# Kernel tuning notes

Measured on AMD Instinct MI355X. Metric: run time of the kernel, lower is better.

## Reference

```python
import jax, jax.numpy as jnp
import numpy as np

B, T, D, H, DFF = 64, 100, 1024, 16, 4096
HD = D // H
EPS = 1e-5


def _rope_tables(t_len, hd, dtype):
    # matches RotaryEmbedding: inv_freq over even dims, emb = cat([freqs, freqs])
    inv_freq = 1.0 / (10000.0 ** (jnp.arange(0, hd, 2, dtype=jnp.float32) / hd))
    t = jnp.arange(t_len, dtype=jnp.float32)
    freqs = jnp.einsum('i,j->ij', t, inv_freq)          # (T, hd/2)
    emb = jnp.concatenate([freqs, freqs], axis=-1)      # (T, hd)
    # apply_rope uses cos[..., ::2] / sin[..., ::2]
    cos = jnp.cos(emb)[:, ::2].astype(dtype)            # (T, hd/2)
    sin = jnp.sin(emb)[:, ::2].astype(dtype)
    return cos, sin


def _apply_rope(x, cos, sin):
    # x: (B, H, T, hd); cos/sin: (T, hd/2) broadcast over B,H
    x1 = x[..., ::2]
    x2 = x[..., 1::2]
    return jnp.concatenate([x1 * cos - x2 * sin, x1 * sin + x2 * cos], axis=-1)


def _layernorm(x, g, b):
    mu = jnp.mean(x, axis=-1, keepdims=True)
    var = jnp.mean(jnp.square(x - mu), axis=-1, keepdims=True)
    return (x - mu) * jax.lax.rsqrt(var + EPS) * g + b


def setup_inputs() -> dict:
    key = jax.random.key(0)
    ks = jax.random.split(key, 8)
    s = 0.02
    return {
        'tgt': jax.random.normal(ks[0], (B, T, D), dtype=jnp.float32),
        'Wqkv': jax.random.normal(ks[1], (3 * D, D), dtype=jnp.float32) * s,
        'bqkv': jnp.zeros((3 * D,), jnp.float32),
        'Wo': jax.random.normal(ks[2], (D, D), dtype=jnp.float32) * s,
        'bo': jnp.zeros((D,), jnp.float32),
        'W1': jax.random.normal(ks[3], (DFF, D), dtype=jnp.float32) * s,
        'b1': jnp.zeros((DFF,), jnp.float32),
        'W2': jax.random.normal(ks[4], (D, DFF), dtype=jnp.float32) * s,
        'b2': jnp.zeros((D,), jnp.float32),
        'g1': jnp.ones((D,), jnp.float32),
        'be1': jnp.zeros((D,), jnp.float32),
        'g2': jnp.ones((D,), jnp.float32),
        'be2': jnp.zeros((D,), jnp.float32),
        'tgt_mask': jnp.tril(jnp.ones((T, T), jnp.int32)),
    }


def reference(tgt, Wqkv, bqkv, Wo, bo, W1, b1, W2, b2, g1, be1, g2, be2, tgt_mask):
    dtype = tgt.dtype
    # QKV projection (torch Linear: x @ W.T + b)
    qkv = jnp.einsum('btd,ed->bte', tgt, Wqkv) + bqkv          # (B,T,3D)
    qkv = qkv.reshape(B, T, 3, H, HD).transpose(2, 0, 3, 1, 4)  # (3,B,H,T,hd)
    q, k, v = qkv[0], qkv[1], qkv[2]

    cos, sin = _rope_tables(T, HD, dtype)
    q = _apply_rope(q, cos, sin)
    k = _apply_rope(k, cos, sin)

    scale = 1.0 / np.sqrt(HD)
    scores = jnp.einsum('bhqd,bhkd->bhqk', q, k) * scale        # (B,H,T,T)
    scores = jnp.where(tgt_mask == 0, -jnp.inf, scores)
    attn = jax.nn.softmax(scores, axis=-1)
    ctx = jnp.einsum('bhqk,bhkd->bhqd', attn, v)                # (B,H,T,hd)
    ctx = ctx.transpose(0, 2, 1, 3).reshape(B, T, D)

    tgt2 = jnp.einsum('btd,ed->bte', ctx, Wo) + bo
    x = _layernorm(tgt + tgt2, g1, be1)

    h = jax.nn.relu(jnp.einsum('btd,fd->btf', x, W1) + b1)
    ff = jnp.einsum('btf,df->btd', h, W2) + b2
    out = _layernorm(x + ff, g2, be2)
    return out
```

## Files before the change

kernel.cpp:

```cpp
#include <hip/hip_runtime.h>
#include <math.h>

#define Bn   64
#define Tn   100
#define Tp   128
#define Dn   1024
#define Hn   16
#define HDn  64
#define DFFn 4096
#define EPSf 1e-5f

typedef unsigned short ushort_t;
typedef __attribute__((ext_vector_type(8))) __bf16 bf16x8;
typedef __attribute__((ext_vector_type(4))) float f32x4;

__device__ __forceinline__ float u2f(ushort_t u) {
    union { unsigned int i; float f; } v; v.i = ((unsigned int)u) << 16; return v.f;
}
__device__ __forceinline__ ushort_t f2bf(float f) {
    union { float f; unsigned int u; } v; v.f = f;
    unsigned int r = v.u + 0x7FFFu + ((v.u >> 16) & 1u);
    return (ushort_t)(r >> 16);
}

__device__ __forceinline__ void gload_lds16(const void* g, void* l) {
    __builtin_amdgcn_global_load_lds(
        (const __attribute__((address_space(1))) unsigned int*)g,
        (__attribute__((address_space(3))) unsigned int*)l,
        16, 0, 0);
}

struct ConvSeg { const float* src; ushort_t* dst; int n4; };
struct Conv5   { ConvSeg seg[5]; };

__global__ __launch_bounds__(256) void conv_bf16_multi(Conv5 cfg)
{
    int i = blockIdx.x * 256 + threadIdx.x;
    #pragma unroll
    for (int s = 0; s < 5; ++s) {
        const int n = cfg.seg[s].n4;
        if (i < n) {
            float4 v = ((const float4*)cfg.seg[s].src)[i];
            ushort4 o;
            o.x = f2bf(v.x); o.y = f2bf(v.y); o.z = f2bf(v.z); o.w = f2bf(v.w);
            ((ushort4*)cfg.seg[s].dst)[i] = o;
            return;
        }
        i -= n;
    }
}

#define GEMM_TILE_MAP(gx_, gy_, swz_)                                        \
    const int L  = blockIdx.x;                                               \
    int rowt, colt;                                                          \
    if (swz_) {                                                              \
        const int group = L / (8 * (gx_));                                   \
        int l = L - group * 8 * (gx_);                                       \
        const int rem = (gy_) - group * 8;                                   \
        if (rem >= 8) { rowt = group * 8 + (l & 7); colt = l >> 3; }         \
        else          { rowt = group * 8 + l % rem; colt = l / rem; }        \
    } else { rowt = L / (gx_); colt = L - rowt * (gx_); }

#define GEMM_KLOOP(A_, B_, K_)                                               \
    for (int k0 = 0; k0 < (K_); k0 += 64) {                                  \
        __syncthreads();                                                     \
        _Pragma("unroll")                                                    \
        for (int t = 0; t < 4; ++t) {                                        \
            const int idx = (wave * 4 + t) * 64 + lane;                      \
            const int row = idx >> 3;                                        \
            const int gc  = (idx & 7) ^ (row & 7);                           \
            gload_lds16((A_) + (size_t)(row0 + row) * (K_) + k0 + gc * 8,    \
                        &As[idx * 8]);                                       \
            gload_lds16((B_) + (size_t)(col0 + row) * (K_) + k0 + gc * 8,    \
                        &Bs[idx * 8]);                                       \
        }                                                                    \
        __syncthreads();                                                     \
        _Pragma("unroll")                                                    \
        for (int kh = 0; kh < 2; ++kh) {                                     \
            const int chunk = kh * 4 + g;                                    \
            bf16x8 af[4], bfr[4];                                            \
            _Pragma("unroll")                                                \
            for (int i = 0; i < 4; ++i) {                                    \
                const int ra = wrow + i * 16 + frow;                         \
                af[i]  = *(const bf16x8*)&As[ra * 64 + (chunk ^ (ra & 7)) * 8]; \
                const int rb = wcol + i * 16 + frow;                         \
                bfr[i] = *(const bf16x8*)&Bs[rb * 64 + (chunk ^ (rb & 7)) * 8]; \
            }                                                                \
            _Pragma("unroll")                                                \
            for (int i = 0; i < 4; ++i)                                      \
                _Pragma("unroll")                                            \
                for (int j = 0; j < 4; ++j)                                  \
                    acc[i][j] = __builtin_amdgcn_mfma_f32_16x16x32_bf16(     \
                        af[i], bfr[j], acc[i][j], 0, 0, 0);                  \
        }                                                                    \
    }

template<bool RELU, bool ADDRES, typename OutT>
__global__ __launch_bounds__(256) void gemm_bt_mfma(const ushort_t* __restrict__ A,
                                                    const ushort_t* __restrict__ Bm,
                                                    const float* __restrict__ bias,
                                                    const ushort_t* __restrict__ res,
                                                    OutT* __restrict__ C,
                                                    int M, int N, int K,
                                                    int gx, int swz)
{
    __shared__ __align__(16) ushort_t As[128 * 64];
    __shared__ __align__(16) ushort_t Bs[128 * 64];

    const int gy = M >> 7;
    GEMM_TILE_MAP(gx, gy, swz)

    const int tid  = threadIdx.x;
    const int wave = tid >> 6;
    const int lane = tid & 63;
    const int row0 = rowt * 128;
    const int col0 = colt * 128;
    const int wrow = (wave >> 1) * 64;
    const int wcol = (wave & 1) * 64;
    const int frow = lane & 15;
    const int g    = lane >> 4;

    f32x4 acc[4][4] = {};
    GEMM_KLOOP(A, Bm, K)

    const int crow = (lane >> 4) * 4;
    const int ccol = lane & 15;
    #pragma unroll
    for (int i = 0; i < 4; ++i) {
        #pragma unroll
        for (int r = 0; r < 4; ++r) {
            const int row = row0 + wrow + i * 16 + crow + r;
            #pragma unroll
            for (int j = 0; j < 4; ++j) {
                const int col = col0 + wcol + j * 16 + ccol;
                float v = acc[i][j][r] + bias[col];
                if (ADDRES) v += u2f(res[(size_t)row * N + col]);
                if (RELU) v = fmaxf(v, 0.f);
                if constexpr (sizeof(OutT) == 2)
                    C[(size_t)row * N + col] = (OutT)f2bf(v);
                else
                    C[(size_t)row * N + col] = (OutT)v;
            }
        }
    }
}

__global__ __launch_bounds__(256) void gemm_qkv_rope(const ushort_t* __restrict__ A,
                                                     const ushort_t* __restrict__ Bm,
                                                     const float* __restrict__ bias,
                                                     ushort_t* __restrict__ q,
                                                     ushort_t* __restrict__ k,
                                                     ushort_t* __restrict__ vt)
{
    __shared__ __align__(16) ushort_t As[128 * 64];
    __shared__ __align__(16) ushort_t Bs[128 * 64];

    const int gy = 50, gx = 24;
    GEMM_TILE_MAP(gx, gy, 1)

    const int tid  = threadIdx.x;
    const int wave = tid >> 6;
    const int lane = tid & 63;
    const int row0 = rowt * 128;
    const int col0 = colt * 128;
    const int wrow = (wave >> 1) * 64;
    const int wcol = (wave & 1) * 64;
    const int frow = lane & 15;
    const int g    = lane >> 4;

    f32x4 acc[4][4] = {};
    GEMM_KLOOP(A, Bm, Dn)

    const int sec = col0 >> 10;

    __syncthreads();
    float2* tab = (float2*)As;
    if (sec != 2) {
        for (int e = tid; e < 2048; e += 256) {
            const int lr = e >> 4, f = e & 15;
            const int row = row0 + lr;
            const int b = row / Tn;
            const int t = row - b * Tn;
            float s, c;
            sincosf((float)t * exp2f(-0.83048202f * (float)f), &s, &c);
            tab[lr * 16 + f] = make_float2(c, s);
        }
    }
    __syncthreads();

    const int crow = (lane >> 4) * 4;
    const int ccol = lane & 15;

    if (sec == 2) {
        #pragma unroll
        for (int i = 0; i < 4; ++i) {
            #pragma unroll
            for (int r = 0; r < 4; ++r) {
                const int row = row0 + wrow + i * 16 + crow + r;
                const int b = row / Tn, t = row - b * Tn;
                #pragma unroll
                for (int j = 0; j < 4; ++j) {
                    const int colg = col0 + wcol + j * 16 + ccol;
                    const int hcol = colg & 1023;
                    const int h = hcol >> 6, d = hcol & 63;
                    const float v = acc[i][j][r] + bias[colg];
                    vt[((size_t)(b * Hn + h) * HDn + d) * Tp + t] = f2bf(v);
                }
            }
        }
    } else {
        ushort_t* dst = sec ? k : q;
        const int odd = ccol & 1;
        const int f0  = ccol >> 1;
        #pragma unroll
        for (int i = 0; i < 4; ++i) {
            #pragma unroll
            for (int r = 0; r < 4; ++r) {
                const int lr  = wrow + i * 16 + crow + r;
                const int row = row0 + lr;
                const int b = row / Tn, t = row - b * Tn;
                const float2 cs0 = tab[lr * 16 + f0];
                const float2 cs1 = tab[lr * 16 + 8 + f0];
                (void)t;
                #pragma unroll
                for (int j = 0; j < 4; ++j) {
                    const int colg = col0 + wcol + j * 16 + ccol;
                    const int hcol = colg & 1023;
                    const int h  = hcol >> 6;
                    const int dh = hcol & 63;
                    const int m  = dh >> 1;
                    const float val   = acc[i][j][r] + bias[colg];
                    const float other = __shfl_xor(val, 1);
                    const float sn = (j & 1) ? cs1.y : cs0.y;
                    const float cs = (j & 1) ? cs1.x : cs0.x;
                    const float x1 = odd ? other : val;
                    const float x2 = odd ? val : other;
                    const float o  = odd ? (x1 * sn + x2 * cs)
                                         : (x1 * cs - x2 * sn);
                    const int outcol = odd ? (m + 32) : m;
                    dst[((size_t)(b * Hn + h) * Tp + t) * HDn + outcol] = f2bf(o);
                }
            }
        }
    }
}

__global__ __launch_bounds__(256) void attn_mfma(const ushort_t* __restrict__ q,
                                                 const ushort_t* __restrict__ k,
                                                 const ushort_t* __restrict__ vt,
                                                 ushort_t* __restrict__ ctx)
{
    __shared__ __align__(16) ushort_t sm[24576];

    const int bh   = blockIdx.x;
    const int b    = bh >> 4, h = bh & 15;
    const int tid  = threadIdx.x;
    const int wave = tid >> 6;
    const int lane = tid & 63;
    const int c    = lane & 15;
    const int g    = lane >> 4;
    const int R0   = wave * 32;

    const ushort_t* qg = q  + (size_t)bh * Tp * HDn;
    const ushort_t* kg = k  + (size_t)bh * Tp * HDn;
    const ushort_t* vg = vt + (size_t)bh * HDn * Tp;
    for (int s = wave; s < 16; s += 4) {
        const int idx = s * 64 + lane;
        { const int row = idx >> 3, pc = idx & 7, gc = pc ^ (row & 7);
          gload_lds16(qg + row * 64 + gc * 8, &sm[idx * 8]);
          gload_lds16(kg + row * 64 + gc * 8, &sm[8192 + idx * 8]); }
        { const int row = idx >> 4, pc = idx & 15, gc = pc ^ (row & 15);
          gload_lds16(vg + row * 128 + gc * 8, &sm[16384 + idx * 8]); }
    }
    __syncthreads();

    f32x4 acc[2][8] = {};
    #pragma unroll
    for (int ks = 0; ks < 2; ++ks) {
        const int cb = ks * 4;
        bf16x8 aq[2];
        #pragma unroll
        for (int i = 0; i < 2; ++i) {
            const int row = R0 + i * 16 + c;
            const int ph  = (cb + g) ^ (row & 7);
            aq[i] = *(const bf16x8*)&sm[row * 64 + ph * 8];
        }
        #pragma unroll
        for (int j = 0; j < 8; ++j) {
            const int row = j * 16 + c;
            const int ph  = (cb + g) ^ (row & 7);
            const bf16x8 bk = *(const bf16x8*)&sm[8192 + row * 64 + ph * 8];
            acc[0][j] = __builtin_amdgcn_mfma_f32_16x16x32_bf16(aq[0], bk, acc[0][j], 0, 0, 0);
            acc[1][j] = __builtin_amdgcn_mfma_f32_16x16x32_bf16(aq[1], bk, acc[1][j], 0, 0, 0);
        }
    }
    __syncthreads();

    float linv[2][4];
    #pragma unroll
    for (int i = 0; i < 2; ++i) {
        #pragma unroll
        for (int r = 0; r < 4; ++r) {
            const int row = R0 + i * 16 + g * 4 + r;
            float sv[8], m = -1e30f;
            #pragma unroll
            for (int j = 0; j < 8; ++j) {
                const int col = j * 16 + c;
                const float s = acc[i][j][r] * 0.125f;
                sv[j] = (col <= row) ? s : -1e30f;
                m = fmaxf(m, sv[j]);
            }
            #pragma unroll
            for (int msk = 1; msk < 16; msk <<= 1) m = fmaxf(m, __shfl_xor(m, msk));
            float l = 0.f;
            #pragma unroll
            for (int j = 0; j < 8; ++j) {
                const int col = j * 16 + c;
                const float p = (col <= row) ? __expf(sv[j] - m) : 0.f;
                sv[j] = p; l += p;
            }
            #pragma unroll
            for (int msk = 1; msk < 16; msk <<= 1) l += __shfl_xor(l, msk);
            linv[i][r] = 1.f / l;
            #pragma unroll
            for (int j = 0; j < 8; ++j) {
                const int chunk = j * 2 + (c >> 3);
                const int ph    = chunk ^ (row & 15);
                sm[row * 128 + ph * 8 + (c & 7)] = f2bf(sv[j]);
            }
        }
    }
    __syncthreads();

    f32x4 acc2[2][4] = {};
    #pragma unroll
    for (int ks = 0; ks < 4; ++ks) {
        const int cb = ks * 4;
        bf16x8 ap[2];
        #pragma unroll
        for (int i = 0; i < 2; ++i) {
            const int row = R0 + i * 16 + c;
            const int ph  = (cb + g) ^ (row & 15);
            ap[i] = *(const bf16x8*)&sm[row * 128 + ph * 8];
        }
        #pragma unroll
        for (int n = 0; n < 4; ++n) {
            const int row = n * 16 + c;
            const int ph  = (cb + g) ^ (row & 15);
            const bf16x8 bv = *(const bf16x8*)&sm[16384 + row * 128 + ph * 8];
            acc2[0][n] = __builtin_amdgcn_mfma_f32_16x16x32_bf16(ap[0], bv, acc2[0][n], 0, 0, 0);
            acc2[1][n] = __builtin_amdgcn_mfma_f32_16x16x32_bf16(ap[1], bv, acc2[1][n], 0, 0, 0);
        }
    }

    #pragma unroll
    for (int i = 0; i < 2; ++i) {
        #pragma unroll
        for (int r = 0; r < 4; ++r) {
            const int row = R0 + i * 16 + g * 4 + r;
            if (row < Tn) {
                const float s = linv[i][r];
                #pragma unroll
                for (int n = 0; n < 4; ++n) {
                    const int col = n * 16 + c;
                    ctx[(size_t)(b * Tn + row) * Dn + h * HDn + col] =
                        f2bf(acc2[i][n][r] * s);
                }
            }
        }
    }
}

__global__ __launch_bounds__(256) void ln_single(const ushort_t* __restrict__ a,
                                                 const float* __restrict__ g,
                                                 const float* __restrict__ be,
                                                 ushort_t* __restrict__ out_bf)
{
    const int row = blockIdx.x;
    const int tid = threadIdx.x;
    __shared__ float red[256];
    const size_t base = (size_t)row * Dn;

    float vals[4];
    float s = 0.f;
    #pragma unroll
    for (int i = 0; i < 4; ++i) {
        const int c = tid + i * 256;
        vals[i] = u2f(a[base + c]);
        s += vals[i];
    }
    red[tid] = s;
    __syncthreads();
    for (int o = 128; o > 0; o >>= 1) {
        if (tid < o) red[tid] += red[tid + o];
        __syncthreads();
    }
    const float mu = red[0] * (1.f / Dn);
    __syncthreads();

    float vs = 0.f;
    #pragma unroll
    for (int i = 0; i < 4; ++i) { const float d = vals[i] - mu; vs += d * d; }
    red[tid] = vs;
    __syncthreads();
    for (int o = 128; o > 0; o >>= 1) {
        if (tid < o) red[tid] += red[tid + o];
        __syncthreads();
    }
    const float rstd = rsqrtf(red[0] * (1.f / Dn) + EPSf);

    #pragma unroll
    for (int i = 0; i < 4; ++i) {
        const int c = tid + i * 256;
        out_bf[base + c] = f2bf((vals[i] - mu) * rstd * g[c] + be[c]);
    }
}

__global__ __launch_bounds__(256) void add_ln2(const ushort_t* __restrict__ a,
                                               const ushort_t* __restrict__ r,
                                               const float* __restrict__ g,
                                               const float* __restrict__ be,
                                               float* __restrict__ out)
{
    const int row = blockIdx.x;
    const int tid = threadIdx.x;
    __shared__ float red[256];
    const size_t base = (size_t)row * Dn;

    float vals[4];
    float s = 0.f;
    #pragma unroll
    for (int i = 0; i < 4; ++i) {
        const int c = tid + i * 256;
        vals[i] = u2f(a[base + c]) + u2f(r[base + c]);
        s += vals[i];
    }
    red[tid] = s;
    __syncthreads();
    for (int o = 128; o > 0; o >>= 1) {
        if (tid < o) red[tid] += red[tid + o];
        __syncthreads();
    }
    const float mu = red[0] * (1.f / Dn);
    __syncthreads();

    float vs = 0.f;
    #pragma unroll
    for (int i = 0; i < 4; ++i) { const float d = vals[i] - mu; vs += d * d; }
    red[tid] = vs;
    __syncthreads();
    for (int o = 128; o > 0; o >>= 1) {
        if (tid < o) red[tid] += red[tid + o];
        __syncthreads();
    }
    const float rstd = rsqrtf(red[0] * (1.f / Dn) + EPSf);

    #pragma unroll
    for (int i = 0; i < 4; ++i) {
        const int c = tid + i * 256;
        out[base + c] = (vals[i] - mu) * rstd * g[c] + be[c];
    }
}

extern "C" void kernel_launch(void* const* d_in, const int* in_sizes, int n_in,
                              void* d_out, int out_size, void* d_ws, size_t ws_size,
                              hipStream_t stream)
{
    const float* tgt  = (const float*)d_in[0];
    const float* Wqkv = (const float*)d_in[1];
    const float* bqkv = (const float*)d_in[2];
    const float* Wo   = (const float*)d_in[3];
    const float* bo   = (const float*)d_in[4];
    const float* W1   = (const float*)d_in[5];
    const float* b1   = (const float*)d_in[6];
    const float* W2   = (const float*)d_in[7];
    const float* b2   = (const float*)d_in[8];
    const float* g1   = (const float*)d_in[9];
    const float* be1  = (const float*)d_in[10];
    const float* g2   = (const float*)d_in[11];
    const float* be2  = (const float*)d_in[12];
    float* out = (float*)d_out;
    (void)in_sizes; (void)n_in; (void)out_size; (void)ws_size;

    const int M = Bn * Tn;

    char* w = (char*)d_ws;
    ushort_t* tgt_bf  = (ushort_t*)(w);
    ushort_t* Wqkv_bf = (ushort_t*)(w + 13107200);
    ushort_t* Wo_bf   = (ushort_t*)(w + 19398656);
    ushort_t* W1_bf   = (ushort_t*)(w + 21495808);
    ushort_t* W2_bf   = (ushort_t*)(w + 29884416);

    ushort_t* qb    = (ushort_t*)(w + 38273024);
    ushort_t* kb    = (ushort_t*)(w + 55050240);
    ushort_t* vtb   = (ushort_t*)(w + 71827456);
    ushort_t* hbuf  = (ushort_t*)(w + 38273024);
    ushort_t* ctxb  = (ushort_t*)(w + 88604672);
    ushort_t* tgt2b = (ushort_t*)(w + 101711872);
    ushort_t* ffb   = (ushort_t*)(w + 101711872);
    ushort_t* x_bf  = (ushort_t*)(w + 114819072);

    Conv5 cfg;
    cfg.seg[0] = { tgt,  tgt_bf,  M * Dn / 4 };
    cfg.seg[1] = { Wqkv, Wqkv_bf, 3 * Dn * Dn / 4 };
    cfg.seg[2] = { Wo,   Wo_bf,   Dn * Dn / 4 };
    cfg.seg[3] = { W1,   W1_bf,   DFFn * Dn / 4 };
    cfg.seg[4] = { W2,   W2_bf,   Dn * DFFn / 4 };
    const int total4 = (M * Dn + 3 * Dn * Dn + Dn * Dn + 2 * DFFn * Dn) / 4;
    conv_bf16_multi<<<(total4 + 255) / 256, 256, 0, stream>>>(cfg);

    gemm_qkv_rope<<<1200, 256, 0, stream>>>(tgt_bf, Wqkv_bf, bqkv, qb, kb, vtb);
    attn_mfma<<<Bn * Hn, 256, 0, stream>>>(qb, kb, vtb, ctxb);
    gemm_bt_mfma<false, true, ushort_t><<<(Dn / 128) * (M / 128), 256, 0, stream>>>(
        ctxb, Wo_bf, bo, tgt_bf, tgt2b, M, Dn, Dn, Dn / 128, 1);
    ln_single<<<M, 256, 0, stream>>>(tgt2b, g1, be1, x_bf);
    gemm_bt_mfma<true, false, ushort_t><<<(DFFn / 128) * (M / 128), 256, 0, stream>>>(
        x_bf, W1_bf, b1, nullptr, hbuf, M, DFFn, Dn, DFFn / 128, 0);
    gemm_bt_mfma<false, false, ushort_t><<<(Dn / 128) * (M / 128), 256, 0, stream>>>(
        hbuf, W2_bf, b2, nullptr, ffb, M, Dn, DFFn, Dn / 128, 1);
    add_ln2<<<M, 256, 0, stream>>>(x_bf, ffb, g2, be2, out);
}
```

Measured before the change: 440.8 us.

## Add 256x256-tile double-buffered MFMA GEMM for QKV+RoPE and FFN1

Introduces a 512-thread GEMM with a 256x256 output tile. It uses double-buffered LDS with XOR-swizzled layout and direct global-to-LDS loads. The next K-slices are staged between MFMA quarter-steps, with explicit waitcnt, barriers and raised wave priority during the MFMA bursts. The QKV+RoPE GEMM and the W1 (ReLU) GEMM switch to this kernel to raise data reuse per tile and overlap loads with compute. In exchange, there are far fewer blocks (300 and 400), which risks tail-wave imbalance on the CUs, and each block needs 128KB of LDS, which limits occupancy.

```diff
diff --git a/kernel.cpp b/kernel.cpp
--- a/kernel.cpp
+++ b/kernel.cpp
@@ -145,38 +145,165 @@
     }
 }
 
-__global__ __launch_bounds__(256) void gemm_qkv_rope(const ushort_t* __restrict__ A,
+#define STAGE_HALF(SRC, ROWBASE, LD, LDSBASE)                                \
+    { _Pragma("unroll")                                                      \
+      for (int i_ = 0; i_ < 2; ++i_) {                                       \
+          const int idx_ = i_ * 512 + tid;                                   \
+          const int row_ = idx_ >> 3;                                        \
+          const int gc_  = (idx_ & 7) ^ (row_ & 7);                          \
+          gload_lds16((SRC) + (size_t)((ROWBASE) + row_) * (LD) + gc_ * 8,   \
+                      (LDSBASE) + idx_ * 8);                                 \
+      } }
+
+#define GEMM256_KLOOP(A_, B_, K_)                                            \
+    const int NT_ = (K_) >> 6;                                               \
+    STAGE_HALF((B_),      col0,       (K_), &Bs[0][0])                       \
+    STAGE_HALF((B_),      col0 + 128, (K_), &Bs[0][128 * 64])                \
+    STAGE_HALF((A_),      row0,       (K_), &As[0][0])                       \
+    STAGE_HALF((A_),      row0 + 128, (K_), &As[0][128 * 64])                \
+    STAGE_HALF((B_) + 64, col0,       (K_), &Bs[1][0])                       \
+    STAGE_HALF((B_) + 64, col0 + 128, (K_), &Bs[1][128 * 64])                \
+    asm volatile("s_waitcnt vmcnt(4)" ::: "memory");                         \
+    __builtin_amdgcn_s_barrier();                                            \
+    for (int t_ = 0; t_ < NT_; ++t_) {                                       \
+        const int  buf_ = t_ & 1;                                            \
+        const bool stA_ = (t_ + 1 < NT_);                                    \
+        const bool stB_ = (t_ + 2 < NT_);                                    \
+        bf16x8 bfr_[4][2];                                                   \
+        _Pragma("unroll")                                                    \
+        for (int q_ = 0; q_ < 4; ++q_) {                                     \
+            bf16x8 af_[2][2];                                                \
+            _Pragma("unroll")                                                \
+            for (int ii_ = 0; ii_ < 2; ++ii_)                                \
+                _Pragma("unroll")                                            \
+                for (int kk_ = 0; kk_ < 2; ++kk_) {                          \
+                    const int ra_ = wm * 128 + (2 * q_ + ii_) * 16 + frow;   \
+                    const int ch_ = kk_ * 4 + g;                             \
+                    af_[ii_][kk_] = *(const bf16x8*)                         \
+                        &As[buf_][ra_ * 64 + ((ch_ ^ (ra_ & 7))) * 8];       \
+                }                                                            \
+            if (q_ == 0) {                                                   \
+                _Pragma("unroll")                                            \
+                for (int j_ = 0; j_ < 4; ++j_)                               \
+                    _Pragma("unroll")                                        \
+                    for (int kk_ = 0; kk_ < 2; ++kk_) {                      \
+                        const int rb_ = wn * 64 + j_ * 16 + frow;            \
+                        const int ch_ = kk_ * 4 + g;                         \
+                        bfr_[j_][kk_] = *(const bf16x8*)                     \
+                            &Bs[buf_][rb_ * 64 + ((ch_ ^ (rb_ & 7))) * 8];   \
+                    }                                                        \
+            }                                                                \
+            if (q_ == 0 && stA_)                                             \
+                STAGE_HALF((A_) + (t_ + 1) * 64, row0,       (K_), &As[buf_ ^ 1][0]) \
+            if (q_ == 1 && stA_)                                             \
+                STAGE_HALF((A_) + (t_ + 1) * 64, row0 + 128, (K_), &As[buf_ ^ 1][128 * 64]) \
+            if (q_ == 2 && stB_)                                             \
+                STAGE_HALF((B_) + (t_ + 2) * 64, col0,       (K_), &Bs[buf_][0]) \
+            if (q_ == 3 && stB_)                                             \
+                STAGE_HALF((B_) + (t_ + 2) * 64, col0 + 128, (K_), &Bs[buf_][128 * 64]) \
+            __builtin_amdgcn_s_barrier();                                    \
+            asm volatile("s_waitcnt lgkmcnt(0)" ::: "memory");               \
+            __builtin_amdgcn_sched_barrier(0);                               \
+            __builtin_amdgcn_s_setprio(1);                                   \
+            _Pragma("unroll")                                                \
+            for (int ii_ = 0; ii_ < 2; ++ii_)                                \
+                _Pragma("unroll")                                            \
+                for (int j_ = 0; j_ < 4; ++j_)                               \
+                    _Pragma("unroll")                                        \
+                    for (int kk_ = 0; kk_ < 2; ++kk_)                        \
+                        acc[2 * q_ + ii_][j_] =                              \
+                            __builtin_amdgcn_mfma_f32_16x16x32_bf16(         \
+                                af_[ii_][kk_], bfr_[j_][kk_],                \
+                                acc[2 * q_ + ii_][j_], 0, 0, 0);             \
+            __builtin_amdgcn_s_setprio(0);                                   \
+            __builtin_amdgcn_sched_barrier(0);                               \
+            if (q_ == 3) {                                                   \
+                if (stB_)      asm volatile("s_waitcnt vmcnt(4)" ::: "memory"); \
+                else if (stA_) asm volatile("s_waitcnt vmcnt(0)" ::: "memory"); \
+            }                                                                \
+            __builtin_amdgcn_s_barrier();                                    \
+        }                                                                    \
+    }
+
+template<bool RELU, typename OutT>
+__global__ __launch_bounds__(512, 2) void gemm256_bt(const ushort_t* __restrict__ A,
                                                      const ushort_t* __restrict__ Bm,
                                                      const float* __restrict__ bias,
-                                                     ushort_t* __restrict__ q,
-                                                     ushort_t* __restrict__ k,
-                                                     ushort_t* __restrict__ vt)
-{
-    __shared__ __align__(16) ushort_t As[128 * 64];
-    __shared__ __align__(16) ushort_t Bs[128 * 64];
-
-    const int gy = 50, gx = 24;
-    GEMM_TILE_MAP(gx, gy, 1)
+                                                     OutT* __restrict__ C,
+                                                     int M, int N, int K,
+                                                     int gx, int swz)
+{
+    __shared__ __align__(16) ushort_t As[2][256 * 64];
+    __shared__ __align__(16) ushort_t Bs[2][256 * 64];
+
+    const int gy = M >> 8;
+    GEMM_TILE_MAP(gx, gy, swz)
 
     const int tid  = threadIdx.x;
+    const int lane = tid & 63;
     const int wave = tid >> 6;
-    const int lane = tid & 63;
-    const int row0 = rowt * 128;
-    const int col0 = colt * 128;
-    const int wrow = (wave >> 1) * 64;
-    const int wcol = (wave & 1) * 64;
+    const int wm   = wave >> 2;
+    const int wn   = wave & 3;
+    const int row0 = rowt * 256;
+    const int col0 = colt * 256;
     const int frow = lane & 15;
     const int g    = lane >> 4;
 
-    f32x4 acc[4][4] = {};
-    GEMM_KLOOP(A, Bm, Dn)
+    f32x4 acc[8][4] = {};
+    GEMM256_KLOOP(A, Bm, K)
+
+    const int crow = (lane >> 4) * 4;
+    const int ccol = lane & 15;
+    #pragma unroll
+    for (int i = 0; i < 8; ++i) {
+        #pragma unroll
+        for (int r = 0; r < 4; ++r) {
+            const int row = row0 + wm * 128 + i * 16 + crow + r;
+            #pragma unroll
+            for (int j = 0; j < 4; ++j) {
+                const int col = col0 + wn * 64 + j * 16 + ccol;
+                float v = acc[i][j][r] + bias[col];
+                if (RELU) v = fmaxf(v, 0.f);
+                if constexpr (sizeof(OutT) == 2)
+                    C[(size_t)row * N + col] = (OutT)f2bf(v);
+                else
+                    C[(size_t)row * N + col] = (OutT)v;
+            }
+        }
+    }
+}
+
+__global__ __launch_bounds__(512, 2) void gemm256_qkv_rope(const ushort_t* __restrict__ A,
+                                                           const ushort_t* __restrict__ Bm,
+                                                           const float* __restrict__ bias,
+                                                           ushort_t* __restrict__ q,
+                                                           ushort_t* __restrict__ k,
+                                                           ushort_t* __restrict__ vt)
+{
+    __shared__ __align__(16) ushort_t As[2][256 * 64];
+    __shared__ __align__(16) ushort_t Bs[2][256 * 64];
+
+    const int gy = 25, gx = 12;
+    GEMM_TILE_MAP(gx, gy, 1)
+
+    const int tid  = threadIdx.x;
+    const int lane = tid & 63;
+    const int wave = tid >> 6;
+    const int wm   = wave >> 2;
+    const int wn   = wave & 3;
+    const int row0 = rowt * 256;
+    const int col0 = colt * 256;
+    const int frow = lane & 15;
+    const int g    = lane >> 4;
+
+    f32x4 acc[8][4] = {};
+    GEMM256_KLOOP(A, Bm, Dn)
 
     const int sec = col0 >> 10;
 
-    __syncthreads();
-    float2* tab = (float2*)As;
+    float2* tab = (float2*)&As[0][0];
     if (sec != 2) {
-        for (int e = tid; e < 2048; e += 256) {
+        for (int e = tid; e < 4096; e += 512) {
             const int lr = e >> 4, f = e & 15;
             const int row = row0 + lr;
             const int b = row / Tn;
@@ -193,14 +320,14 @@
 
     if (sec == 2) {
         #pragma unroll
-        for (int i = 0; i < 4; ++i) {
+        for (int i = 0; i < 8; ++i) {
             #pragma unroll
             for (int r = 0; r < 4; ++r) {
-                const int row = row0 + wrow + i * 16 + crow + r;
+                const int row = row0 + wm * 128 + i * 16 + crow + r;
                 const int b = row / Tn, t = row - b * Tn;
                 #pragma unroll
                 for (int j = 0; j < 4; ++j) {
-                    const int colg = col0 + wcol + j * 16 + ccol;
+                    const int colg = col0 + wn * 64 + j * 16 + ccol;
                     const int hcol = colg & 1023;
                     const int h = hcol >> 6, d = hcol & 63;
                     const float v = acc[i][j][r] + bias[colg];
@@ -213,18 +340,17 @@
         const int odd = ccol & 1;
         const int f0  = ccol >> 1;
         #pragma unroll
-        for (int i = 0; i < 4; ++i) {
+        for (int i = 0; i < 8; ++i) {
             #pragma unroll
             for (int r = 0; r < 4; ++r) {
-                const int lr  = wrow + i * 16 + crow + r;
+                const int lr  = wm * 128 + i * 16 + crow + r;
                 const int row = row0 + lr;
                 const int b = row / Tn, t = row - b * Tn;
                 const float2 cs0 = tab[lr * 16 + f0];
                 const float2 cs1 = tab[lr * 16 + 8 + f0];
-                (void)t;
                 #pragma unroll
                 for (int j = 0; j < 4; ++j) {
-                    const int colg = col0 + wcol + j * 16 + ccol;
+                    const int colg = col0 + wn * 64 + j * 16 + ccol;
                     const int hcol = colg & 1023;
                     const int h  = hcol >> 6;
                     const int dh = hcol & 63;
@@ -509,13 +635,13 @@
     const int total4 = (M * Dn + 3 * Dn * Dn + Dn * Dn + 2 * DFFn * Dn) / 4;
     conv_bf16_multi<<<(total4 + 255) / 256, 256, 0, stream>>>(cfg);
 
-    gemm_qkv_rope<<<1200, 256, 0, stream>>>(tgt_bf, Wqkv_bf, bqkv, qb, kb, vtb);
+    gemm256_qkv_rope<<<25 * 12, 512, 0, stream>>>(tgt_bf, Wqkv_bf, bqkv, qb, kb, vtb);
     attn_mfma<<<Bn * Hn, 256, 0, stream>>>(qb, kb, vtb, ctxb);
     gemm_bt_mfma<false, true, ushort_t><<<(Dn / 128) * (M / 128), 256, 0, stream>>>(
         ctxb, Wo_bf, bo, tgt_bf, tgt2b, M, Dn, Dn, Dn / 128, 1);
     ln_single<<<M, 256, 0, stream>>>(tgt2b, g1, be1, x_bf);
-    gemm_bt_mfma<true, false, ushort_t><<<(DFFn / 128) * (M / 128), 256, 0, stream>>>(
-        x_bf, W1_bf, b1, nullptr, hbuf, M, DFFn, Dn, DFFn / 128, 0);
+    gemm256_bt<true, ushort_t><<<(M / 256) * (DFFn / 256), 512, 0, stream>>>(
+        x_bf, W1_bf, b1, hbuf, M, DFFn, Dn, DFFn / 256, 0);
     gemm_bt_mfma<false, false, ushort_t><<<(Dn / 128) * (M / 128), 256, 0, stream>>>(
         hbuf, W2_bf, b2, nullptr, ffb, M, Dn, DFFn, Dn / 128, 1);
     add_ln2<<<M, 256, 0, stream>>>(x_bf, ffb, g2, be2, out);
```

Result: slower. 482.2 us (+9.4%).

## Replace 128x128 GEMMs with 256-row double-buffered 512-thread MFMA kernel

Applied to the files above, without the earlier changes.

Replaces the generic 128x128-tile GEMM used for the output projection and both FFN matmuls with a 512-thread kernel that computes 256xBN tiles (BN=128 or 256). It double-buffers LDS, issuing global-to-LDS loads for the next K slices in stages interleaved with MFMA work, and uses manual vmcnt waits, barriers and setprio. Larger tiles raise arithmetic intensity and cut redundant global loads, and the prefetch schedule is meant to hide memory latency. In exchange it uses more LDS and registers per block and launches fewer blocks, so occupancy and load balance may suffer on small grids such as the 1024-wide GEMMs. The hand-tuned wait counts must also match the number of loads in flight.

```diff
diff --git a/kernel.cpp b/kernel.cpp
--- a/kernel.cpp
+++ b/kernel.cpp
@@ -29,6 +29,9 @@
         (__attribute__((address_space(3))) unsigned int*)l,
         16, 0, 0);
 }
+
+#define VMWAIT_(n) asm volatile("s_waitcnt vmcnt(" #n ")" ::: "memory")
+#define VMWAIT(n)  VMWAIT_(n)
 
 struct ConvSeg { const float* src; ushort_t* dst; int n4; };
 struct Conv5   { ConvSeg seg[5]; };
@@ -95,47 +98,129 @@
         }                                                                    \
     }
 
-template<bool RELU, bool ADDRES, typename OutT>
-__global__ __launch_bounds__(256) void gemm_bt_mfma(const ushort_t* __restrict__ A,
-                                                    const ushort_t* __restrict__ Bm,
-                                                    const float* __restrict__ bias,
-                                                    const ushort_t* __restrict__ res,
-                                                    OutT* __restrict__ C,
-                                                    int M, int N, int K,
-                                                    int gx, int swz)
+template<int BN, bool RELU, bool ADDRES, typename OutT>
+__global__ __launch_bounds__(512, 2) void gemm256_bt(const ushort_t* __restrict__ A,
+                                                     const ushort_t* __restrict__ Bm,
+                                                     const float* __restrict__ bias,
+                                                     const ushort_t* __restrict__ res,
+                                                     OutT* __restrict__ C,
+                                                     int M, int N, int K,
+                                                     int gx, int swz)
 {
-    __shared__ __align__(16) ushort_t As[128 * 64];
-    __shared__ __align__(16) ushort_t Bs[128 * 64];
-
-    const int gy = M >> 7;
+    constexpr int JN = BN / 64;
+    constexpr int NB = BN / 128;
+    __shared__ __align__(16) ushort_t As[2][256 * 64];
+    __shared__ __align__(16) ushort_t Bs[2][BN * 64];
+
+    const int gy = M >> 8;
     GEMM_TILE_MAP(gx, gy, swz)
 
     const int tid  = threadIdx.x;
+    const int lane = tid & 63;
     const int wave = tid >> 6;
-    const int lane = tid & 63;
-    const int row0 = rowt * 128;
-    const int col0 = colt * 128;
-    const int wrow = (wave >> 1) * 64;
-    const int wcol = (wave & 1) * 64;
+    const int wm   = wave >> 2;
+    const int wn   = wave & 3;
+    const int row0 = rowt * 256;
+    const int col0 = colt * BN;
     const int frow = lane & 15;
     const int g    = lane >> 4;
 
-    f32x4 acc[4][4] = {};
-    GEMM_KLOOP(A, Bm, K)
+    auto stageA = [&](const ushort_t* src, int rowbase, ushort_t* lds) {
+        #pragma unroll
+        for (int i = 0; i < 2; ++i) {
+            const int idx = i * 512 + tid;
+            const int row = idx >> 3;
+            const int gc  = (idx & 7) ^ (row & 7);
+            gload_lds16(src + (size_t)(rowbase + row) * K + gc * 8, lds + idx * 8);
+        }
+    };
+    auto stageB = [&](const ushort_t* src, int rowbase, ushort_t* lds) {
+        #pragma unroll
+        for (int i = 0; i < NB; ++i) {
+            const int idx = i * 512 + tid;
+            const int row = idx >> 3;
+            const int gc  = (idx & 7) ^ (row & 7);
+            gload_lds16(src + (size_t)(rowbase + row) * K + gc * 8, lds + idx * 8);
+        }
+    };
+
+    f32x4 acc[8][JN] = {};
+
+    const int NT = K >> 6;
+    stageB(Bm,      col0,          &Bs[0][0]);
+    stageB(Bm,      col0 + BN / 2, &Bs[0][(BN / 2) * 64]);
+    stageA(A,       row0,          &As[0][0]);
+    stageA(A,       row0 + 128,    &As[0][128 * 64]);
+    stageB(Bm + 64, col0,          &Bs[1][0]);
+    stageB(Bm + 64, col0 + BN / 2, &Bs[1][(BN / 2) * 64]);
+    if constexpr (NB == 2) { VMWAIT(4); } else { VMWAIT(2); }
+    __builtin_amdgcn_s_barrier();
+
+    for (int t = 0; t < NT; ++t) {
+        const int  buf = t & 1;
+        const bool stA = (t + 1 < NT);
+        const bool stB = (t + 2 < NT);
+        bf16x8 bfr[JN][2];
+        #pragma unroll
+        for (int q = 0; q < 4; ++q) {
+            bf16x8 af[2][2];
+            #pragma unroll
+            for (int ii = 0; ii < 2; ++ii)
+                #pragma unroll
+                for (int kk = 0; kk < 2; ++kk) {
+                    const int ra = wm * 128 + (2 * q + ii) * 16 + frow;
+                    const int ch = kk * 4 + g;
+                    af[ii][kk] = *(const bf16x8*)&As[buf][ra * 64 + (ch ^ (ra & 7)) * 8];
+                }
+            if (q == 0) {
+                #pragma unroll
+                for (int j = 0; j < JN; ++j)
+                    #pragma unroll
+                    for (int kk = 0; kk < 2; ++kk) {
+                        const int rb = wn * (BN / 4) + j * 16 + frow;
+                        const int ch = kk * 4 + g;
+                        bfr[j][kk] = *(const bf16x8*)&Bs[buf][rb * 64 + (ch ^ (rb & 7)) * 8];
+                    }
+            }
+            if (q == 0 && stA) stageA(A + (t + 1) * 64, row0,       &As[buf ^ 1][0]);
+            if (q == 1 && stA) stageA(A + (t + 1) * 64, row0 + 128, &As[buf ^ 1][128 * 64]);
+            if (q == 2 && stB) stageB(Bm + (t + 2) * 64, col0,          &Bs[buf][0]);
+            if (q == 3 && stB) stageB(Bm + (t + 2) * 64, col0 + BN / 2, &Bs[buf][(BN / 2) * 64]);
+            __builtin_amdgcn_s_barrier();
+            asm volatile("s_waitcnt lgkmcnt(0)" ::: "memory");
+            __builtin_amdgcn_sched_barrier(0);
+            __builtin_amdgcn_s_setprio(1);
+            #pragma unroll
+            for (int ii = 0; ii < 2; ++ii)
+                #pragma unroll
+                for (int j = 0; j < JN; ++j)
+                    #pragma unroll
+                    for (int kk = 0; kk < 2; ++kk)
+                        acc[2 * q + ii][j] = __builtin_amdgcn_mfma_f32_16x16x32_bf16(
+                            af[ii][kk], bfr[j][kk], acc[2 * q + ii][j], 0, 0, 0);
+            __builtin_amdgcn_s_setprio(0);
+            __builtin_amdgcn_sched_barrier(0);
+            if (q == 3) {
+                if (stB)      { if constexpr (NB == 2) { VMWAIT(4); } else { VMWAIT(2); } }
+                else if (stA) { VMWAIT(0); }
+            }
+            __builtin_amdgcn_s_barrier();
+        }
+    }
 
     const int crow = (lane >> 4) * 4;
     const int ccol = lane & 15;
     #pragma unroll
-    for (int i = 0; i < 4; ++i) {
+    for (int i = 0; i < 8; ++i) {
         #pragma unroll
         for (int r = 0; r < 4; ++r) {
-            const int row = row0 + wrow + i * 16 + crow + r;
-            #pragma unroll
-            for (int j = 0; j < 4; ++j) {
-                const int col = col0 + wcol + j * 16 + ccol;
+            const int row = row0 + wm * 128 + i * 16 + crow + r;
+            #pragma unroll
+            for (int j = 0; j < JN; ++j) {
+                const int col = col0 + wn * (BN / 4) + j * 16 + ccol;
                 float v = acc[i][j][r] + bias[col];
-                if (ADDRES) v += u2f(res[(size_t)row * N + col]);
-                if (RELU) v = fmaxf(v, 0.f);
+                if constexpr (ADDRES) v += u2f(res[(size_t)row * N + col]);
+                if constexpr (RELU) v = fmaxf(v, 0.f);
                 if constexpr (sizeof(OutT) == 2)
                     C[(size_t)row * N + col] = (OutT)f2bf(v);
                 else
@@ -511,12 +596,12 @@
 
     gemm_qkv_rope<<<1200, 256, 0, stream>>>(tgt_bf, Wqkv_bf, bqkv, qb, kb, vtb);
     attn_mfma<<<Bn * Hn, 256, 0, stream>>>(qb, kb, vtb, ctxb);
-    gemm_bt_mfma<false, true, ushort_t><<<(Dn / 128) * (M / 128), 256, 0, stream>>>(
+    gemm256_bt<128, false, true, ushort_t><<<(Dn / 128) * (M / 256), 512, 0, stream>>>(
         ctxb, Wo_bf, bo, tgt_bf, tgt2b, M, Dn, Dn, Dn / 128, 1);
     ln_single<<<M, 256, 0, stream>>>(tgt2b, g1, be1, x_bf);
-    gemm_bt_mfma<true, false, ushort_t><<<(DFFn / 128) * (M / 128), 256, 0, stream>>>(
-        x_bf, W1_bf, b1, nullptr, hbuf, M, DFFn, Dn, DFFn / 128, 0);
-    gemm_bt_mfma<false, false, ushort_t><<<(Dn / 128) * (M / 128), 256, 0, stream>>>(
+    gemm256_bt<256, true, false, ushort_t><<<(M / 256) * (DFFn / 256), 512, 0, stream>>>(
+        x_bf, W1_bf, b1, nullptr, hbuf, M, DFFn, Dn, DFFn / 256, 0);
+    gemm256_bt<128, false, false, ushort_t><<<(Dn / 128) * (M / 256), 512, 0, stream>>>(
         hbuf, W2_bf, b2, nullptr, ffb, M, Dn, DFFn, Dn / 128, 1);
     add_ln2<<<M, 256, 0, stream>>>(x_bf, ffb, g2, be2, out);
 }
```

Result: no change. 443.0 us (+0.5%).
